# Kernel tuning notes

Hardware: AMD Instinct MI355X
Metric: run time of the kernel (lower is better)

The kernel has to match this reference:

```python
import jax, jax.numpy as jnp
import numpy as np

FEAT = 172
EDGE = 172
TIME = 172
DM = FEAT + EDGE + TIME  # 516
H = 2
DK = DM // H  # 258
B = 4096
N = 64


def setup_inputs() -> dict:
    key = jax.random.key(0)
    ks = jax.random.split(key, 20)
    s = 0.05
    inp = {
        "src": jax.random.normal(ks[0], (B, FEAT), jnp.float32),
        "src_t": jax.random.normal(ks[1], (B, 1, TIME), jnp.float32),
        "seq": jax.random.normal(ks[2], (B, N, FEAT), jnp.float32),
        "seq_t": jax.random.normal(ks[3], (B, N, TIME), jnp.float32),
        "seq_e": jax.random.normal(ks[4], (B, N, EDGE), jnp.float32),
        "mask": jnp.zeros((B, N), jnp.bool_),
        # attention params (torch Linear weight layout: [out, in])
        "Wq": jax.random.normal(ks[5], (H * DK, DM), jnp.float32) * s,
        "Wk": jax.random.normal(ks[6], (H * DK, DM), jnp.float32) * s,
        "Wv": jax.random.normal(ks[7], (H * DK, DM), jnp.float32) * s,
        "w_map": jax.random.normal(ks[8], (1, 2 * DK), jnp.float32) * s,
        "Wfc": jax.random.normal(ks[9], (DM, H * DK), jnp.float32) * s,
        "bfc": jnp.zeros((DM,), jnp.float32),
        "ln_g": jnp.ones((DM,), jnp.float32),
        "ln_b": jnp.zeros((DM,), jnp.float32),
        # merger params
        "W1": jax.random.normal(ks[10], (FEAT, DM + FEAT), jnp.float32) * s,
        "b1": jnp.zeros((FEAT,), jnp.float32),
        "W2": jax.random.normal(ks[11], (FEAT, FEAT), jnp.float32) * s,
        "b2": jnp.zeros((FEAT,), jnp.float32),
    }
    return inp


def reference(src, src_t, seq, seq_t, seq_e, mask,
              Wq, Wk, Wv, w_map, Wfc, bfc, ln_g, ln_b, W1, b1, W2, b2):
    b = src.shape[0]
    # build q/k inputs: q = [src, 0, src_t], k = [seq, seq_e, seq_t]
    src_ext = src[:, None, :]                                    # [B,1,F]
    q_in = jnp.concatenate([src_ext, jnp.zeros_like(src_ext), src_t], axis=2)  # [B,1,DM]
    k_in = jnp.concatenate([seq, seq_e, seq_t], axis=2)          # [B,N,DM]

    qp = (q_in @ Wq.T).reshape(b, 1, H, DK)                      # [B,1,H,dk]
    kp = (k_in @ Wk.T).reshape(b, N, H, DK)                      # [B,N,H,dk]
    vp = (k_in @ Wv.T).reshape(b, N, H, DK)                      # [B,N,H,dv]

    # map-based scorer: Linear(2*dk -> 1, no bias) on concat(q,k) == w1.q + w2.k
    w1, w2 = w_map[0, :DK], w_map[0, DK:]
    sq = jnp.einsum('bqhd,d->bhq', qp, w1)                       # [B,H,1]
    sk = jnp.einsum('bkhd,d->bhk', kp, w2)                       # [B,H,N]
    scores = sq[..., :, None] + sk[:, :, None, :]                # [B,H,1,N]

    scores = jnp.where(mask[:, None, None, :], jnp.float32(-1e10), scores)
    attn = jax.nn.softmax(scores, axis=-1)                       # [B,H,1,N]

    ctx = jnp.einsum('bhqk,bkhd->bqhd', attn, vp).reshape(b, 1, H * DK)
    h = jax.nn.leaky_relu(ctx @ Wfc.T + bfc, negative_slope=0.2)  # [B,1,DM]

    x = h + q_in  # residual
    mu = jnp.mean(x, axis=-1, keepdims=True)
    var = jnp.var(x, axis=-1, keepdims=True)
    out = (x - mu) / jnp.sqrt(var + 1e-5) * ln_g + ln_b          # LayerNorm
    out = out[:, 0, :]                                           # [B,DM]

    # MergeLayer
    m = jnp.concatenate([out, src], axis=1)                      # [B,DM+F]
    hm = jax.nn.relu(m @ W1.T + b1)
    final = hm @ W2.T + b2                                       # [B,F]

    # attn as original layout: [n_head*B, N] (head-major, len_q squeezed)
    attn_out = attn[:, :, 0, :].transpose(1, 0, 2).reshape(H * b, N)
    return (final, attn_out)
```

## Files before the change

kernel.cpp:

```cpp
#include <hip/hip_runtime.h>
#include <cstddef>

#define B_    4096
#define N_    64
#define FEAT_ 172
#define DM_   516
#define DK_   258

#define OFF_U      0
#define OFF_WVP    1032
#define OFF_WFCP   (1032 + 266256)
#define OFF_W1P    (1032 + 2*266256)
#define OFF_W2P    (1032 + 2*266256 + 118336)
#define OFF_CTXIN  (1032 + 2*266256 + 118336 + 29584)

__global__ __launch_bounds__(256) void prep_kernel(
    const float* __restrict__ Wk, const float* __restrict__ wmap,
    const float* __restrict__ Wv, const float* __restrict__ Wfc,
    const float* __restrict__ W1, const float* __restrict__ W2,
    float* __restrict__ ws)
{
  int i = blockIdx.x * 256 + threadIdx.x;
  float*  u    = ws + OFF_U;
  float4* Wvp  = (float4*)(ws + OFF_WVP);
  float4* Wfcp = (float4*)(ws + OFF_WFCP);
  float4* W1p  = (float4*)(ws + OFF_W1P);
  float4* W2p  = (float4*)(ws + OFF_W2P);
  if (i < 66564) {
    int c4 = i / 516, j = i % 516;
    Wvp[i] = *(const float4*)&Wv[(size_t)j*516 + 4*c4];
  } else if (i < 133128) {
    int o = i - 66564; int c4 = o / 516, j = o % 516;
    Wfcp[o] = *(const float4*)&Wfc[(size_t)j*516 + 4*c4];
  } else if (i < 162712) {
    int o = i - 133128; int c4 = o / 172, j = o % 172;
    W1p[o] = *(const float4*)&W1[(size_t)j*688 + 4*c4];
  } else if (i < 170108) {
    int o = i - 162712; int c4 = o / 172, j = o % 172;
    W2p[o] = *(const float4*)&W2[(size_t)j*172 + 4*c4];
  } else if (i < 171140) {
    int o = i - 170108; int h = o / 516, c = o % 516;
    float s = 0.f;
    for (int d = 0; d < 258; ++d)
      s += Wk[(size_t)(h*258 + d)*516 + c] * wmap[258 + d];
    u[o] = s;
  }
}

__global__ __launch_bounds__(256) void attn_kernel(
    const float* __restrict__ seq, const float* __restrict__ seqe,
    const float* __restrict__ seqt, const unsigned char* __restrict__ mask,
    const float* __restrict__ ws, float* __restrict__ ctxin,
    float* __restrict__ attn_out)
{
  __shared__ float buf[16*516];
  __shared__ float u_l[1032];
  __shared__ float p2[32];
  __shared__ float pall[128];
  __shared__ float sinv_l[2];

  const float* u = ws + OFF_U;
  int t = threadIdx.x;
  int b = blockIdx.x;

  for (int i = t; i < 258; i += 256) ((float4*)u_l)[i] = ((const float4*)u)[i];

  float2 a0 = {0.f,0.f}, a1 = {0.f,0.f}, e0 = {0.f,0.f}, e1 = {0.f,0.f};

  const float* g0b = seq  + (size_t)b*64*172;
  const float* g1b = seqe + (size_t)b*64*172;
  const float* g2b = seqt + (size_t)b*64*172;

  int sub = t & 7, pr = t >> 3;
  int hB = pr >> 4, kB = pr & 15;
  int startB = (sub == 0) ? 0 : (16*sub + 1);
  int cntB   = (sub == 0) ? 17 : 16;

  for (int chunk = 0; chunk < 4; ++chunk) {
    int kk0 = chunk*16;
    {
      const float4* g0 = (const float4*)(g0b + (size_t)kk0*172);
      const float4* g1 = (const float4*)(g1b + (size_t)kk0*172);
      const float4* g2 = (const float4*)(g2b + (size_t)kk0*172);
      for (int f = t; f < 688; f += 256) {
        int r = f / 43, c4 = f - r*43;
        float4 v0 = g0[f], v1 = g1[f], v2 = g2[f];
        *(float4*)&buf[r*516 +       c4*4] = v0;
        *(float4*)&buf[r*516 + 172 + c4*4] = v1;
        *(float4*)&buf[r*516 + 344 + c4*4] = v2;
      }
    }
    __syncthreads();
    {
      float s = 0.f;
      const float4* row4 = (const float4*)&buf[kB*516];
      const float4* u4   = (const float4*)&u_l[hB*516];
      for (int ii = 0; ii < cntB; ++ii) {
        float4 a = row4[startB + ii];
        float4 w = u4[startB + ii];
        s += a.x*w.x + a.y*w.y + a.z*w.z + a.w*w.w;
      }
      s += __shfl_xor(s, 1);
      s += __shfl_xor(s, 2);
      s += __shfl_xor(s, 4);
      if (sub == 0) {
        int kk = kk0 + kB;
        float pv = mask[(size_t)b*64 + kk] ? 0.f : expf(s);
        p2[kB*2 + hB] = pv;
        pall[kk*2 + hB] = pv;
      }
    }
    __syncthreads();
    {
      #pragma unroll 4
      for (int k = 0; k < 16; ++k) {
        float2 p = *(const float2*)&p2[k*2];
        float2 v = *(const float2*)&buf[k*516 + 2*t];
        a0.x += p.x*v.x; a0.y += p.x*v.y;
        a1.x += p.y*v.x; a1.y += p.y*v.y;
        if (t < 2) {
          float2 v2 = *(const float2*)&buf[k*516 + 2*(256+t)];
          e0.x += p.x*v2.x; e0.y += p.x*v2.y;
          e1.x += p.y*v2.x; e1.y += p.y*v2.y;
        }
      }
    }
    __syncthreads();
  }
  if (t < 128) {
    int h = t >> 6, k = t & 63;
    float pv = pall[k*2 + h];
    float ssum = pv;
    #pragma unroll
    for (int off = 1; off < 64; off <<= 1) ssum += __shfl_xor(ssum, off);
    attn_out[((size_t)h*B_ + b)*64 + k] = pv / ssum;
    if (k == 0) sinv_l[h] = 1.f / ssum;
  }
  __syncthreads();
  float s0 = sinv_l[0], s1 = sinv_l[1];
  float* cb = ctxin + (size_t)b*1032;
  *(float2*)&cb[2*t]       = make_float2(a0.x*s0, a0.y*s0);
  *(float2*)&cb[516 + 2*t] = make_float2(a1.x*s1, a1.y*s1);
  if (t < 2) {
    *(float2*)&cb[2*(256+t)]       = make_float2(e0.x*s0, e0.y*s0);
    *(float2*)&cb[516 + 2*(256+t)] = make_float2(e1.x*s1, e1.y*s1);
  }
}

__global__ __launch_bounds__(576) void chain_kernel(
    const float* __restrict__ ws, const float* __restrict__ src,
    const float* __restrict__ srct,
    const float* __restrict__ bfc, const float* __restrict__ lng,
    const float* __restrict__ lnb, const float* __restrict__ b1,
    const float* __restrict__ b2, float* __restrict__ finalout)
{
  __shared__ float A[16*1032];
  __shared__ float Ctx[16*516];
  __shared__ float Red[9*16*2];
  __shared__ float MuSig[32];

  const float*  ctxin = ws + OFF_CTXIN;
  const float4* Wvp   = (const float4*)(ws + OFF_WVP);
  const float4* Wfcp  = (const float4*)(ws + OFF_WFCP);
  const float4* W1p   = (const float4*)(ws + OFF_W1P);
  const float4* W2p   = (const float4*)(ws + OFF_W2P);

  int t = threadIdx.x;
  int b0 = blockIdx.x * 16;

  {
    const float4* g = (const float4*)(ctxin + (size_t)b0*1032);
    float4* a4 = (float4*)A;
    for (int f = t; f < 4128; f += 576) a4[f] = g[f];
  }
  __syncthreads();

  int j = t;
  bool actj = (j < 516);
  int hh = (j < 258) ? 0 : 1;
  float acc[16];
  #pragma unroll
  for (int r = 0; r < 16; ++r) acc[r] = 0.f;
  if (actj) {
    const float* Ab = &A[hh*516];
    for (int c4 = 0; c4 < 129; ++c4) {
      float4 w = Wvp[c4*516 + j];
      #pragma unroll
      for (int r = 0; r < 16; ++r) {
        float4 a = *(const float4*)&Ab[r*1032 + 4*c4];
        acc[r] += a.x*w.x + a.y*w.y + a.z*w.z + a.w*w.w;
      }
    }
    #pragma unroll
    for (int r = 0; r < 16; ++r) Ctx[r*516 + j] = acc[r];
  }
  __syncthreads();

  #pragma unroll
  for (int r = 0; r < 16; ++r) acc[r] = 0.f;
  if (actj) {
    for (int c4 = 0; c4 < 129; ++c4) {
      float4 w = Wfcp[c4*516 + j];
      #pragma unroll
      for (int r = 0; r < 16; ++r) {
        float4 a = *(const float4*)&Ctx[r*516 + 4*c4];
        acc[r] += a.x*w.x + a.y*w.y + a.z*w.z + a.w*w.w;
      }
    }
  }
  float bfcj = actj ? bfc[j] : 0.f;
  float x[16];
  #pragma unroll
  for (int r = 0; r < 16; ++r) {
    float v = acc[r] + bfcj;
    v = (v > 0.f) ? v : 0.2f*v;
    float q = 0.f;
    if (j < 172)                        q = src[(size_t)(b0+r)*172 + j];
    else if (j >= 344 && j < 516)       q = srct[(size_t)(b0+r)*172 + (j - 344)];
    x[r] = actj ? (v + q) : 0.f;
  }
  int wv = t >> 6, lane = t & 63;
  #pragma unroll
  for (int r = 0; r < 16; ++r) {
    float s = x[r], q = x[r]*x[r];
    #pragma unroll
    for (int off = 1; off < 64; off <<= 1) { s += __shfl_xor(s, off); q += __shfl_xor(q, off); }
    if (lane == 0) { Red[(wv*16 + r)*2] = s; Red[(wv*16 + r)*2 + 1] = q; }
  }
  __syncthreads();
  if (t < 16) {
    float s = 0.f, q = 0.f;
    for (int w = 0; w < 9; ++w) { s += Red[(w*16 + t)*2]; q += Red[(w*16 + t)*2 + 1]; }
    float mu  = s * (1.f/516.f);
    float var = q * (1.f/516.f) - mu*mu;
    MuSig[t*2]   = mu;
    MuSig[t*2+1] = rsqrtf(var + 1e-5f);
  }
  __syncthreads();
  float* M = A;
  if (actj) {
    float lg = lng[j], lb = lnb[j];
    #pragma unroll
    for (int r = 0; r < 16; ++r)
      M[r*688 + j] = (x[r] - MuSig[r*2]) * MuSig[r*2+1] * lg + lb;
  }
  for (int i = t; i < 2752; i += 576) {
    int r = i / 172, c = i - r*172;
    M[r*688 + 516 + c] = src[(size_t)(b0 + r)*172 + c];
  }
  __syncthreads();

  {
    float acc3[16];
    #pragma unroll
    for (int r = 0; r < 16; ++r) acc3[r] = 0.f;
    if (actj) {
      int j3 = t % 172, seg = t / 172;
      int c4lo = (seg == 0) ? 0  : ((seg == 1) ? 58  : 115);
      int c4hi = (seg == 0) ? 58 : ((seg == 1) ? 115 : 172);
      for (int c4 = c4lo; c4 < c4hi; ++c4) {
        float4 w = W1p[c4*172 + j3];
        #pragma unroll
        for (int r = 0; r < 16; ++r) {
          float4 a = *(const float4*)&M[r*688 + 4*c4];
          acc3[r] += a.x*w.x + a.y*w.y + a.z*w.z + a.w*w.w;
        }
      }
      float* P3 = Ctx;
      #pragma unroll
      for (int r = 0; r < 16; ++r) P3[(seg*16 + r)*172 + j3] = acc3[r];
    }
  }
  __syncthreads();
  float* Hm = A;
  for (int i = t; i < 2752; i += 576) {
    int r = i / 172, c = i - r*172;
    float v = Ctx[r*172 + c] + Ctx[(16 + r)*172 + c] + Ctx[(32 + r)*172 + c] + b1[c];
    Hm[r*172 + c] = (v > 0.f) ? v : 0.f;
  }
  __syncthreads();

  if (t < 172) {
    float acc4[16];
    #pragma unroll
    for (int r = 0; r < 16; ++r) acc4[r] = 0.f;
    for (int c4 = 0; c4 < 43; ++c4) {
      float4 w = W2p[c4*172 + t];
      #pragma unroll
      for (int r = 0; r < 16; ++r) {
        float4 a = *(const float4*)&Hm[r*172 + 4*c4];
        acc4[r] += a.x*w.x + a.y*w.y + a.z*w.z + a.w*w.w;
      }
    }
    float bb = b2[t];
    #pragma unroll
    for (int r = 0; r < 16; ++r)
      finalout[(size_t)(b0 + r)*172 + t] = acc4[r] + bb;
  }
}

extern "C" void kernel_launch(void* const* d_in, const int* in_sizes, int n_in,
                              void* d_out, int out_size, void* d_ws, size_t ws_size,
                              hipStream_t stream) {
  (void)in_sizes; (void)n_in; (void)out_size; (void)ws_size;
  const float* src  = (const float*)d_in[0];
  const float* srct = (const float*)d_in[1];
  const float* seq  = (const float*)d_in[2];
  const float* seqt = (const float*)d_in[3];
  const float* seqe = (const float*)d_in[4];
  const unsigned char* mask = (const unsigned char*)d_in[5];
  const float* Wk   = (const float*)d_in[7];
  const float* Wv   = (const float*)d_in[8];
  const float* wmap = (const float*)d_in[9];
  const float* Wfc  = (const float*)d_in[10];
  const float* bfc  = (const float*)d_in[11];
  const float* lng  = (const float*)d_in[12];
  const float* lnb  = (const float*)d_in[13];
  const float* W1   = (const float*)d_in[14];
  const float* b1   = (const float*)d_in[15];
  const float* W2   = (const float*)d_in[16];
  const float* b2   = (const float*)d_in[17];

  float* ws = (float*)d_ws;
  float* out = (float*)d_out;
  float* attn_out = out + (size_t)B_*FEAT_;
  float* ctxin = ws + OFF_CTXIN;

  prep_kernel <<<669, 256, 0, stream>>>(Wk, wmap, Wv, Wfc, W1, W2, ws);
  attn_kernel <<<B_, 256, 0, stream>>>(seq, seqe, seqt, mask, ws, ctxin, attn_out);
  chain_kernel<<<B_/16, 576, 0, stream>>>(ws, src, srct, bfc, lng, lnb, b1, b2, out);
}
```

Before: 774.6 us.

## Fold Wv into Wfc and run post-attention chain with bf16 MFMA

Precomputes the combined per-head Wfc·Wv matrix in a prep kernel, so the separate value projection GEMM disappears. The three dense stages of the chain kernel (combined projection, W1, W2) become bf16 MFMA 16x16x32 tiles, with weights pre-swizzled into fragment layout. The aim is to cut the FP32 FMA work and the shared-memory traffic of the old scalar chain. Activations and weights are rounded to bf16, which lowers precision, and the prep step now costs an extra O(DM^3)-sized weight multiply per call.

New measurement: 667.5 us. 13.8% less time.

```diff
diff --git a/kernel.cpp b/kernel.cpp
--- a/kernel.cpp
+++ b/kernel.cpp
@@ -2,48 +2,108 @@
 #include <cstddef>
 
 #define B_    4096
-#define N_    64
 #define FEAT_ 172
-#define DM_   516
-#define DK_   258
 
 #define OFF_U      0
-#define OFF_WVP    1032
-#define OFF_WFCP   (1032 + 266256)
-#define OFF_W1P    (1032 + 2*266256)
-#define OFF_W2P    (1032 + 2*266256 + 118336)
-#define OFF_CTXIN  (1032 + 2*266256 + 118336 + 29584)
-
-__global__ __launch_bounds__(256) void prep_kernel(
+#define OFF_WCS    1032
+#define OFF_W1S    (1032 + 304128)
+#define OFF_W2S    (1032 + 304128 + 67584)
+#define OFF_CTXIN  (1032 + 304128 + 67584 + 18432)
+
+typedef __attribute__((ext_vector_type(8))) short short8;
+typedef __attribute__((ext_vector_type(4))) float f32x4;
+
+__device__ inline unsigned short f2bf(float f) {
+  union { float f; unsigned u; } v; v.f = f;
+  unsigned r = v.u + 0x7FFFu + ((v.u >> 16) & 1u);
+  return (unsigned short)(r >> 16);
+}
+
+__global__ __launch_bounds__(256) void zero_wcs(float* __restrict__ ws) {
+  int i = blockIdx.x * 256 + threadIdx.x;
+  float4* p = (float4*)(ws + OFF_WCS);
+  p[i] = make_float4(0.f, 0.f, 0.f, 0.f);
+}
+
+__global__ __launch_bounds__(256) void prep_u(
     const float* __restrict__ Wk, const float* __restrict__ wmap,
-    const float* __restrict__ Wv, const float* __restrict__ Wfc,
+    float* __restrict__ ws) {
+  int i = blockIdx.x * 256 + threadIdx.x;
+  if (i >= 1032) return;
+  int h = i / 516, c = i % 516;
+  float s = 0.f;
+  for (int d = 0; d < 258; ++d)
+    s += Wk[(size_t)(h*258 + d)*516 + c] * wmap[258 + d];
+  ws[OFF_U + i] = s;
+}
+
+__global__ __launch_bounds__(256) void prep_wcomb(
+    const float* __restrict__ Wfc, const float* __restrict__ Wv,
+    float* __restrict__ ws) {
+  int blk = blockIdx.x;
+  int j0 = (blk >> 1) * 4, h = blk & 1;
+  int t = threadIdx.x;
+  unsigned short* Wcs = (unsigned short*)(ws + OFF_WCS);
+  float s0[4] = {0,0,0,0}, s1[4] = {0,0,0,0}, s2[4] = {0,0,0,0};
+  for (int d = 0; d < 258; ++d) {
+    const float* wv = Wv + (size_t)(h*258 + d)*516;
+    float v0 = wv[t], v1 = wv[256 + t];
+    float v2 = (t < 4) ? wv[512 + t] : 0.f;
+    #pragma unroll
+    for (int jj = 0; jj < 4; ++jj) {
+      float f = Wfc[(size_t)(j0 + jj)*516 + h*258 + d];
+      s0[jj] += f*v0; s1[jj] += f*v1; s2[jj] += f*v2;
+    }
+  }
+  #pragma unroll
+  for (int jj = 0; jj < 4; ++jj) {
+    int j = j0 + jj;
+    int tile = j >> 4, jlow = j & 15;
+    int k;
+    k = h*516 + t;
+    Wcs[(((tile*33 + (k>>5))*64 + ((k>>3)&3)*16 + jlow) << 3) + (k&7)] = f2bf(s0[jj]);
+    k = h*516 + 256 + t;
+    Wcs[(((tile*33 + (k>>5))*64 + ((k>>3)&3)*16 + jlow) << 3) + (k&7)] = f2bf(s1[jj]);
+    if (t < 4) {
+      k = h*516 + 512 + t;
+      Wcs[(((tile*33 + (k>>5))*64 + ((k>>3)&3)*16 + jlow) << 3) + (k&7)] = f2bf(s2[jj]);
+    }
+  }
+}
+
+__global__ __launch_bounds__(256) void prep_w1w2(
     const float* __restrict__ W1, const float* __restrict__ W2,
-    float* __restrict__ ws)
-{
-  int i = blockIdx.x * 256 + threadIdx.x;
-  float*  u    = ws + OFF_U;
-  float4* Wvp  = (float4*)(ws + OFF_WVP);
-  float4* Wfcp = (float4*)(ws + OFF_WFCP);
-  float4* W1p  = (float4*)(ws + OFF_W1P);
-  float4* W2p  = (float4*)(ws + OFF_W2P);
-  if (i < 66564) {
-    int c4 = i / 516, j = i % 516;
-    Wvp[i] = *(const float4*)&Wv[(size_t)j*516 + 4*c4];
-  } else if (i < 133128) {
-    int o = i - 66564; int c4 = o / 516, j = o % 516;
-    Wfcp[o] = *(const float4*)&Wfc[(size_t)j*516 + 4*c4];
-  } else if (i < 162712) {
-    int o = i - 133128; int c4 = o / 172, j = o % 172;
-    W1p[o] = *(const float4*)&W1[(size_t)j*688 + 4*c4];
-  } else if (i < 170108) {
-    int o = i - 162712; int c4 = o / 172, j = o % 172;
-    W2p[o] = *(const float4*)&W2[(size_t)j*172 + 4*c4];
-  } else if (i < 171140) {
-    int o = i - 170108; int h = o / 516, c = o % 516;
-    float s = 0.f;
-    for (int d = 0; d < 258; ++d)
-      s += Wk[(size_t)(h*258 + d)*516 + c] * wmap[258 + d];
-    u[o] = s;
+    float* __restrict__ ws) {
+  int idx = blockIdx.x * 256 + threadIdx.x;
+  unsigned short* W1s = (unsigned short*)(ws + OFF_W1S);
+  unsigned short* W2s = (unsigned short*)(ws + OFF_W2S);
+  if (idx < 16896) {
+    int lane = idx & 63, rest = idx >> 6;
+    int ks = rest % 22, tile = rest / 22;
+    int n = tile*16 + (lane & 15);
+    int k0 = ks*32 + (lane >> 4)*8;
+    union { unsigned short u[8]; uint4 v; } pk;
+    #pragma unroll
+    for (int j = 0; j < 8; ++j) {
+      int k = k0 + j;
+      float v = (n < 172 && k < 688) ? W1[(size_t)n*688 + k] : 0.f;
+      pk.u[j] = f2bf(v);
+    }
+    ((uint4*)W1s)[idx] = pk.v;
+  } else if (idx < 16896 + 4608) {
+    int o = idx - 16896;
+    int lane = o & 63, rest = o >> 6;
+    int ks = rest % 6, tile = rest / 6;
+    int n = tile*16 + (lane & 15);
+    int k0 = ks*32 + (lane >> 4)*8;
+    union { unsigned short u[8]; uint4 v; } pk;
+    #pragma unroll
+    for (int j = 0; j < 8; ++j) {
+      int k = k0 + j;
+      float v = (n < 172 && k < 172) ? W2[(size_t)n*172 + k] : 0.f;
+      pk.u[j] = f2bf(v);
+    }
+    ((uint4*)W2s)[o] = pk.v;
   }
 }
 
@@ -147,155 +207,179 @@
   }
 }
 
-__global__ __launch_bounds__(576) void chain_kernel(
+__global__ __launch_bounds__(256) void chain_kernel(
     const float* __restrict__ ws, const float* __restrict__ src,
-    const float* __restrict__ srct,
-    const float* __restrict__ bfc, const float* __restrict__ lng,
-    const float* __restrict__ lnb, const float* __restrict__ b1,
-    const float* __restrict__ b2, float* __restrict__ finalout)
+    const float* __restrict__ srct, const float* __restrict__ bfc,
+    const float* __restrict__ lng, const float* __restrict__ lnb,
+    const float* __restrict__ b1, const float* __restrict__ b2,
+    float* __restrict__ finalout)
 {
-  __shared__ float A[16*1032];
-  __shared__ float Ctx[16*516];
-  __shared__ float Red[9*16*2];
+  __shared__ __align__(16) unsigned short AM[33*512];
+  __shared__ __align__(16) unsigned short HM[6*512];
+  __shared__ float Red[128];
   __shared__ float MuSig[32];
 
-  const float*  ctxin = ws + OFF_CTXIN;
-  const float4* Wvp   = (const float4*)(ws + OFF_WVP);
-  const float4* Wfcp  = (const float4*)(ws + OFF_WFCP);
-  const float4* W1p   = (const float4*)(ws + OFF_W1P);
-  const float4* W2p   = (const float4*)(ws + OFF_W2P);
+  const unsigned short* Wcs = (const unsigned short*)(ws + OFF_WCS);
+  const unsigned short* W1s = (const unsigned short*)(ws + OFF_W1S);
+  const unsigned short* W2s = (const unsigned short*)(ws + OFF_W2S);
+  const float* ctxin = ws + OFF_CTXIN;
 
   int t = threadIdx.x;
+  int lane = t & 63, w = t >> 6;
   int b0 = blockIdx.x * 16;
+  int cq = lane >> 4;
+  int cl = lane & 15;
 
   {
-    const float4* g = (const float4*)(ctxin + (size_t)b0*1032);
-    float4* a4 = (float4*)A;
-    for (int f = t; f < 4128; f += 576) a4[f] = g[f];
-  }
-  __syncthreads();
-
-  int j = t;
-  bool actj = (j < 516);
-  int hh = (j < 258) ? 0 : 1;
-  float acc[16];
-  #pragma unroll
-  for (int r = 0; r < 16; ++r) acc[r] = 0.f;
-  if (actj) {
-    const float* Ab = &A[hh*516];
-    for (int c4 = 0; c4 < 129; ++c4) {
-      float4 w = Wvp[c4*516 + j];
-      #pragma unroll
-      for (int r = 0; r < 16; ++r) {
-        float4 a = *(const float4*)&Ab[r*1032 + 4*c4];
-        acc[r] += a.x*w.x + a.y*w.y + a.z*w.z + a.w*w.w;
-      }
-    }
-    #pragma unroll
-    for (int r = 0; r < 16; ++r) Ctx[r*516 + j] = acc[r];
-  }
-  __syncthreads();
-
-  #pragma unroll
-  for (int r = 0; r < 16; ++r) acc[r] = 0.f;
-  if (actj) {
-    for (int c4 = 0; c4 < 129; ++c4) {
-      float4 w = Wfcp[c4*516 + j];
-      #pragma unroll
-      for (int r = 0; r < 16; ++r) {
-        float4 a = *(const float4*)&Ctx[r*516 + 4*c4];
-        acc[r] += a.x*w.x + a.y*w.y + a.z*w.z + a.w*w.w;
-      }
-    }
-  }
-  float bfcj = actj ? bfc[j] : 0.f;
-  float x[16];
-  #pragma unroll
-  for (int r = 0; r < 16; ++r) {
-    float v = acc[r] + bfcj;
-    v = (v > 0.f) ? v : 0.2f*v;
-    float q = 0.f;
-    if (j < 172)                        q = src[(size_t)(b0+r)*172 + j];
-    else if (j >= 344 && j < 516)       q = srct[(size_t)(b0+r)*172 + (j - 344)];
-    x[r] = actj ? (v + q) : 0.f;
-  }
-  int wv = t >> 6, lane = t & 63;
-  #pragma unroll
-  for (int r = 0; r < 16; ++r) {
-    float s = x[r], q = x[r]*x[r];
-    #pragma unroll
-    for (int off = 1; off < 64; off <<= 1) { s += __shfl_xor(s, off); q += __shfl_xor(q, off); }
-    if (lane == 0) { Red[(wv*16 + r)*2] = s; Red[(wv*16 + r)*2 + 1] = q; }
-  }
-  __syncthreads();
+    const float4* g = (const float4*)(ctxin + (size_t)b0 * 1032);
+    for (int f = t; f < 4128; f += 256) {
+      int r = f / 258, c4 = f - r*258;
+      float4 v = g[f];
+      int k = c4 * 4;
+      int addr = (((k >> 5)*64 + ((k >> 3) & 3)*16 + r) << 3) + (k & 7);
+      union { unsigned short u[4]; uint2 v2; } pk;
+      pk.u[0] = f2bf(v.x); pk.u[1] = f2bf(v.y); pk.u[2] = f2bf(v.z); pk.u[3] = f2bf(v.w);
+      *(uint2*)&AM[addr] = pk.v2;
+    }
+    for (int i = t; i < 384; i += 256)
+      AM[((32*64 + 16 + (i >> 3)) << 3) + (i & 7)] = 0;
+    for (int i = t; i < 512; i += 256)
+      HM[5*512 + i] = 0;
+  }
+  __syncthreads();
+
+  f32x4 acc[9];
+  #pragma unroll
+  for (int i = 0; i < 9; ++i) acc[i] = (f32x4){0.f, 0.f, 0.f, 0.f};
+  for (int ks = 0; ks < 33; ++ks) {
+    short8 a = *(const short8*)&AM[(ks*64 + lane) << 3];
+    #pragma unroll
+    for (int i = 0; i < 9; ++i) {
+      int tile = w + 4*i;
+      short8 b = *(const short8*)&Wcs[(size_t)((tile*33 + ks)*64 + lane) << 3];
+      acc[i] = __builtin_amdgcn_mfma_f32_16x16x32_bf16(a, b, acc[i], 0, 0, 0);
+    }
+  }
+
+  float x[9][4];
+  float sum[4] = {0,0,0,0}, ssq[4] = {0,0,0,0};
+  #pragma unroll
+  for (int i = 0; i < 9; ++i) {
+    int col = (w + 4*i)*16 + cl;
+    bool valid = col < 516;
+    float bv = valid ? bfc[col] : 0.f;
+    #pragma unroll
+    for (int r = 0; r < 4; ++r) {
+      float v = acc[i][r] + bv;
+      v = (v > 0.f) ? v : 0.2f*v;
+      float qin = 0.f;
+      if (valid) {
+        int row = b0 + cq*4 + r;
+        if (col < 172)       qin = src[(size_t)row*172 + col];
+        else if (col >= 344) qin = srct[(size_t)row*172 + (col - 344)];
+      }
+      float xv = valid ? (v + qin) : 0.f;
+      x[i][r] = xv;
+      sum[r] += xv; ssq[r] += xv*xv;
+    }
+  }
+  #pragma unroll
+  for (int o = 1; o < 16; o <<= 1) {
+    #pragma unroll
+    for (int r = 0; r < 4; ++r) {
+      sum[r] += __shfl_xor(sum[r], o);
+      ssq[r] += __shfl_xor(ssq[r], o);
+    }
+  }
+  if (cl == 0) {
+    #pragma unroll
+    for (int r = 0; r < 4; ++r) {
+      Red[(w*16 + cq*4 + r)*2    ] = sum[r];
+      Red[(w*16 + cq*4 + r)*2 + 1] = ssq[r];
+    }
+  }
+  __syncthreads();
+
   if (t < 16) {
-    float s = 0.f, q = 0.f;
-    for (int w = 0; w < 9; ++w) { s += Red[(w*16 + t)*2]; q += Red[(w*16 + t)*2 + 1]; }
+    float s = 0.f, qq = 0.f;
+    for (int wv = 0; wv < 4; ++wv) { s += Red[(wv*16 + t)*2]; qq += Red[(wv*16 + t)*2 + 1]; }
     float mu  = s * (1.f/516.f);
-    float var = q * (1.f/516.f) - mu*mu;
+    float var = qq * (1.f/516.f) - mu*mu;
     MuSig[t*2]   = mu;
     MuSig[t*2+1] = rsqrtf(var + 1e-5f);
   }
-  __syncthreads();
-  float* M = A;
-  if (actj) {
-    float lg = lng[j], lb = lnb[j];
-    #pragma unroll
-    for (int r = 0; r < 16; ++r)
-      M[r*688 + j] = (x[r] - MuSig[r*2]) * MuSig[r*2+1] * lg + lb;
-  }
-  for (int i = t; i < 2752; i += 576) {
+  for (int i = t; i < 2752; i += 256) {
     int r = i / 172, c = i - r*172;
-    M[r*688 + 516 + c] = src[(size_t)(b0 + r)*172 + c];
-  }
-  __syncthreads();
-
-  {
-    float acc3[16];
-    #pragma unroll
-    for (int r = 0; r < 16; ++r) acc3[r] = 0.f;
-    if (actj) {
-      int j3 = t % 172, seg = t / 172;
-      int c4lo = (seg == 0) ? 0  : ((seg == 1) ? 58  : 115);
-      int c4hi = (seg == 0) ? 58 : ((seg == 1) ? 115 : 172);
-      for (int c4 = c4lo; c4 < c4hi; ++c4) {
-        float4 w = W1p[c4*172 + j3];
-        #pragma unroll
-        for (int r = 0; r < 16; ++r) {
-          float4 a = *(const float4*)&M[r*688 + 4*c4];
-          acc3[r] += a.x*w.x + a.y*w.y + a.z*w.z + a.w*w.w;
-        }
-      }
-      float* P3 = Ctx;
+    int k = 516 + c;
+    AM[(((k >> 5)*64 + ((k >> 3) & 3)*16 + r) << 3) + (k & 7)] =
+        f2bf(src[(size_t)(b0 + r)*172 + c]);
+  }
+  AM[((21*64 + 32 + (t >> 3)) << 3) + (t & 7)] = 0;
+  __syncthreads();
+
+  #pragma unroll
+  for (int i = 0; i < 9; ++i) {
+    int col = (w + 4*i)*16 + cl;
+    if (col < 516) {
+      float lg = lng[col], lb = lnb[col];
       #pragma unroll
-      for (int r = 0; r < 16; ++r) P3[(seg*16 + r)*172 + j3] = acc3[r];
-    }
-  }
-  __syncthreads();
-  float* Hm = A;
-  for (int i = t; i < 2752; i += 576) {
-    int r = i / 172, c = i - r*172;
-    float v = Ctx[r*172 + c] + Ctx[(16 + r)*172 + c] + Ctx[(32 + r)*172 + c] + b1[c];
-    Hm[r*172 + c] = (v > 0.f) ? v : 0.f;
-  }
-  __syncthreads();
-
-  if (t < 172) {
-    float acc4[16];
-    #pragma unroll
-    for (int r = 0; r < 16; ++r) acc4[r] = 0.f;
-    for (int c4 = 0; c4 < 43; ++c4) {
-      float4 w = W2p[c4*172 + t];
+      for (int r = 0; r < 4; ++r) {
+        int row = cq*4 + r;
+        float m = (x[i][r] - MuSig[row*2]) * MuSig[row*2+1] * lg + lb;
+        AM[(((col >> 5)*64 + ((col >> 3) & 3)*16 + row) << 3) + (col & 7)] = f2bf(m);
+      }
+    }
+  }
+  __syncthreads();
+
+  f32x4 accB[3];
+  #pragma unroll
+  for (int i = 0; i < 3; ++i) accB[i] = (f32x4){0.f, 0.f, 0.f, 0.f};
+  for (int ks = 0; ks < 22; ++ks) {
+    short8 a = *(const short8*)&AM[(ks*64 + lane) << 3];
+    #pragma unroll
+    for (int i = 0; i < 3; ++i) {
+      int tile = w + 4*i;
+      short8 b = *(const short8*)&W1s[(size_t)((tile*22 + ks)*64 + lane) << 3];
+      accB[i] = __builtin_amdgcn_mfma_f32_16x16x32_bf16(a, b, accB[i], 0, 0, 0);
+    }
+  }
+  #pragma unroll
+  for (int i = 0; i < 3; ++i) {
+    int col = (w + 4*i)*16 + cl;
+    if (col < 172) {
+      float bb = b1[col];
       #pragma unroll
-      for (int r = 0; r < 16; ++r) {
-        float4 a = *(const float4*)&Hm[r*172 + 4*c4];
-        acc4[r] += a.x*w.x + a.y*w.y + a.z*w.z + a.w*w.w;
-      }
-    }
-    float bb = b2[t];
-    #pragma unroll
-    for (int r = 0; r < 16; ++r)
-      finalout[(size_t)(b0 + r)*172 + t] = acc4[r] + bb;
+      for (int r = 0; r < 4; ++r) {
+        float v = accB[i][r] + bb;
+        v = (v > 0.f) ? v : 0.f;
+        HM[(((col >> 5)*64 + ((col >> 3) & 3)*16 + (cq*4 + r)) << 3) + (col & 7)] = f2bf(v);
+      }
+    }
+  }
+  __syncthreads();
+
+  f32x4 accC[3];
+  #pragma unroll
+  for (int i = 0; i < 3; ++i) accC[i] = (f32x4){0.f, 0.f, 0.f, 0.f};
+  for (int ks = 0; ks < 6; ++ks) {
+    short8 a = *(const short8*)&HM[(ks*64 + lane) << 3];
+    #pragma unroll
+    for (int i = 0; i < 3; ++i) {
+      int tile = w + 4*i;
+      short8 b = *(const short8*)&W2s[(size_t)((tile*6 + ks)*64 + lane) << 3];
+      accC[i] = __builtin_amdgcn_mfma_f32_16x16x32_bf16(a, b, accC[i], 0, 0, 0);
+    }
+  }
+  #pragma unroll
+  for (int i = 0; i < 3; ++i) {
+    int col = (w + 4*i)*16 + cl;
+    if (col < 172) {
+      float bb = b2[col];
+      #pragma unroll
+      for (int r = 0; r < 4; ++r)
+        finalout[(size_t)(b0 + cq*4 + r)*172 + col] = accC[i][r] + bb;
+    }
   }
 }
 
@@ -321,12 +405,15 @@
   const float* W2   = (const float*)d_in[16];
   const float* b2   = (const float*)d_in[17];
 
-  float* ws = (float*)d_ws;
+  float* ws  = (float*)d_ws;
   float* out = (float*)d_out;
   float* attn_out = out + (size_t)B_*FEAT_;
   float* ctxin = ws + OFF_CTXIN;
 
-  prep_kernel <<<669, 256, 0, stream>>>(Wk, wmap, Wv, Wfc, W1, W2, ws);
-  attn_kernel <<<B_, 256, 0, stream>>>(seq, seqe, seqt, mask, ws, ctxin, attn_out);
-  chain_kernel<<<B_/16, 576, 0, stream>>>(ws, src, srct, bfc, lng, lnb, b1, b2, out);
-}
+  zero_wcs   <<<297, 256, 0, stream>>>(ws);
+  prep_u     <<<5,   256, 0, stream>>>(Wk, wmap, ws);
+  prep_wcomb <<<258, 256, 0, stream>>>(Wfc, Wv, ws);
+  prep_w1w2  <<<84,  256, 0, stream>>>(W1, W2, ws);
+  attn_kernel<<<B_,  256, 0, stream>>>(seq, seqe, seqt, mask, ws, ctxin, attn_out);
+  chain_kernel<<<B_/16, 256, 0, stream>>>(ws, src, srct, bfc, lng, lnb, b1, b2, out);
+}
```
